# Optimization experiments

Measured on AMD Instinct MI355X. Metric: run time of the kernel, lower is better.

The kernel has to match this reference:

```python
import jax, jax.numpy as jnp
import numpy as np

D_MODEL = 64     # input_dim // 4
D_INNER = 128    # expand * d_model
D_STATE = 16
D_CONV = 4
DT_RANK = 4      # ceil(d_model / 16)
EPS = 1e-5


def layernorm(x, g, b):
    m = x.mean(-1, keepdims=True)
    v = x.var(-1, keepdims=True)
    return (x - m) * jax.lax.rsqrt(v + EPS) * g + b


def mamba(u, W_in, W_conv, b_conv, W_xproj, W_dt, b_dt, A_log, Dp, W_out):
    # u: [B, L, d_model]
    B, L, _ = u.shape
    xz = u @ W_in.T                              # [B, L, 2*d_inner]
    xi, z = xz[..., :D_INNER], xz[..., D_INNER:]
    # depthwise causal conv1d over L
    xp = jnp.pad(xi, ((0, 0), (D_CONV - 1, 0), (0, 0)))
    xc = b_conv + sum(xp[:, k:k + L, :] * W_conv[:, k] for k in range(D_CONV))
    xc = jax.nn.silu(xc)                         # [B, L, d_inner]
    proj = xc @ W_xproj.T                        # [B, L, dt_rank + 2*d_state]
    dtp = proj[..., :DT_RANK]
    Bm = proj[..., DT_RANK:DT_RANK + D_STATE]    # [B, L, d_state]
    Cm = proj[..., DT_RANK + D_STATE:]           # [B, L, d_state]
    dt = jax.nn.softplus(dtp @ W_dt.T + b_dt)    # [B, L, d_inner]
    A = -jnp.exp(A_log)                          # [d_inner, d_state]
    dA = jnp.exp(dt[..., None] * A)              # [B, L, d_inner, d_state]
    dBx = (dt * xc)[..., None] * Bm[:, :, None, :]

    def step(h, t):
        dA_t, dBx_t, C_t = t
        h = dA_t * h + dBx_t                     # [B, d_inner, d_state]
        return h, jnp.einsum('bds,bs->bd', h, C_t)

    h0 = jnp.zeros((B, D_INNER, D_STATE), u.dtype)
    _, ys = jax.lax.scan(step, h0, (dA.transpose(1, 0, 2, 3),
                                    dBx.transpose(1, 0, 2, 3),
                                    Cm.transpose(1, 0, 2)))
    y = ys.transpose(1, 0, 2) + Dp * xc          # [B, L, d_inner]
    y = y * jax.nn.silu(z)
    return y @ W_out.T                           # [B, L, d_model]


def _forward(x, x1, x2, x3, g1, be1, g2, be2, g3, be3, g4, be4, skip_scale,
             W_in, W_conv, b_conv, W_xproj, W_dt, b_dt, A_log, D, W_out):
    Bb, C = x.shape[:2]
    img_dims = x2.shape[2:]
    mparams = (W_in, W_conv, b_conv, W_xproj, W_dt, b_dt, A_log, D, W_out)

    def branch(inp, g, b):
        xf = inp.reshape(Bb, C, -1).transpose(0, 2, 1)   # [B, L, C]
        xn = layernorm(xf, g, b)
        return mamba(xn, *mparams) + skip_scale * xn

    x_mamba = jnp.concatenate([branch(x, g1, be1), branch(x1, g2, be2),
                               branch(x2, g3, be3), branch(x3, g4, be4)], axis=2)
    out = x_mamba.transpose(0, 2, 1).reshape(Bb, 4 * C, *img_dims)
    return out


def setup_inputs():
    key = jax.random.key(0)
    ks = jax.random.split(key, 12)
    f = lambda k, shp, s=1.0: jax.random.normal(k, shp, dtype=jnp.float32) * s
    inp = {
        'x': f(ks[0], (8, 64, 32, 32)),
        'x1': f(ks[1], (8, 64, 32, 32)),
        'x2': f(ks[2], (8, 64, 32, 32)),
        'x3': f(ks[3], (8, 64, 32, 32)),
        'g1': jnp.ones(64), 'be1': jnp.zeros(64),
        'g2': jnp.ones(64), 'be2': jnp.zeros(64),
        'g3': jnp.ones(64), 'be3': jnp.zeros(64),
        'g4': jnp.ones(64), 'be4': jnp.zeros(64),
        'skip_scale': jnp.ones((1,), jnp.float32),
        'W_in': f(ks[4], (2 * D_INNER, D_MODEL), 0.1),
        'W_conv': f(ks[5], (D_INNER, D_CONV), 0.3),
        'b_conv': jnp.zeros(D_INNER),
        'W_xproj': f(ks[6], (DT_RANK + 2 * D_STATE, D_INNER), 0.1),
        'W_dt': f(ks[7], (D_INNER, DT_RANK), 0.1),
        'b_dt': f(ks[8], (D_INNER,), 0.1),
        'A_log': jnp.log(jnp.tile(jnp.arange(1, D_STATE + 1, dtype=jnp.float32), (D_INNER, 1))),
        'D': jnp.ones(D_INNER),
        'W_out': f(ks[9], (D_MODEL, D_INNER), 0.1),
    }
    return inp


def reference(x, x1, x2, x3, g1, be1, g2, be2, g3, be3, g4, be4, skip_scale,
              W_in, W_conv, b_conv, W_xproj, W_dt, b_dt, A_log, D, W_out):
    return _forward(x, x1, x2, x3, g1, be1, g2, be2, g3, be3, g4, be4, skip_scale,
                    W_in, W_conv, b_conv, W_xproj, W_dt, b_dt, A_log, D, W_out)
```

## Files before the change

### kernel.cpp

```cpp
#include <hip/hip_runtime.h>
#include <hip/hip_bf16.h>

#define L2E 1.4426950408889634f
#define LN2 0.6931471805599453f

__device__ __forceinline__ float fexp2(float x) { return __builtin_amdgcn_exp2f(x); }
__device__ __forceinline__ float flog2(float x) { return __builtin_amdgcn_logf(x); }
__device__ __forceinline__ int uniform(int x) { return __builtin_amdgcn_readfirstlane(x); }
__device__ __forceinline__ float sigmoidf_(float v) { return 1.f / (1.f + fexp2(-v * L2E)); }
__device__ __forceinline__ float softplusf_(float t) {
    return (t > 20.f) ? t : LN2 * flog2(1.f + fexp2(t * L2E));
}

constexpr size_t O_M   = 0;
constexpr size_t O_RS  = 32768;
constexpr size_t O_G   = 65536;
constexpr size_t O_Z   = 4259840;
constexpr size_t O_XC  = 8454144;
constexpr size_t O_BM  = 12648448;
constexpr size_t O_CM  = 13172736;
constexpr size_t O_DTP = 13697024;
constexpr size_t O_HP  = 13828096;

__global__ __launch_bounds__(256) void k1_ln_inproj(
    const float* __restrict__ x0, const float* __restrict__ x1,
    const float* __restrict__ x2, const float* __restrict__ x3,
    const float* __restrict__ win,
    const float* __restrict__ g1, const float* __restrict__ be1,
    const float* __restrict__ g2, const float* __restrict__ be2,
    const float* __restrict__ g3, const float* __restrict__ be3,
    const float* __restrict__ g4, const float* __restrict__ be4,
    float* __restrict__ ws)
{
    __shared__ float sX[64 * 68];
    __shared__ float sW[64 * 68];
    __shared__ float sM[64], sR[64];
    int bid = blockIdx.x;
    int seq = bid >> 6, jb = (bid >> 4) & 3, pb = bid & 15;
    int branch = seq >> 3, b = seq & 7;
    int tid = threadIdx.x;
    int lane = tid & 63;
    int wq = uniform(tid >> 6);
    const float* xin = (branch==0)?x0:(branch==1)?x1:(branch==2)?x2:x3;
    const float* gam = (branch==0)?g1:(branch==1)?g2:(branch==2)?g3:g4;
    const float* bet = (branch==0)?be1:(branch==1)?be2:(branch==2)?be3:be4;
    const float* xb = xin + (size_t)b * 65536;

#pragma unroll
    for (int r = 0; r < 16; ++r) {
        int row = r * 4 + wq;
        sX[row * 68 + lane] = xb[(size_t)row * 1024 + pb * 64 + lane];
        sW[lane * 68 + row] = win[(size_t)(jb * 64 + row) * 64 + lane];
    }
    __syncthreads();
    if (tid < 64) {
        float sum = 0.f, sq = 0.f;
#pragma unroll
        for (int c = 0; c < 64; ++c) {
            float v = sX[c * 68 + tid];
            sum += v; sq += v * v;
        }
        float mean = sum * (1.f/64.f);
        float var  = sq * (1.f/64.f) - mean * mean;
        float rs   = rsqrtf(var + 1e-5f);
        sM[tid] = mean; sR[tid] = rs;
        if (jb == 0) {
            ws[O_M  + (size_t)seq * 1024 + pb * 64 + tid] = mean;
            ws[O_RS + (size_t)seq * 1024 + pb * 64 + tid] = rs;
        }
    }
    __syncthreads();
#pragma unroll
    for (int r = 0; r < 16; ++r) {
        int c = r * 4 + wq;
        float v = sX[c * 68 + lane];
        sX[c * 68 + lane] = (v - sM[lane]) * sR[lane] * gam[c] + bet[c];
    }
    __syncthreads();
    int jt = tid >> 4, pt = tid & 15;
    float acc[4][4];
#pragma unroll
    for (int i = 0; i < 4; ++i)
#pragma unroll
        for (int j = 0; j < 4; ++j) acc[i][j] = 0.f;
    for (int c = 0; c < 64; ++c) {
        float4 wv = *(const float4*)&sW[c * 68 + jt * 4];
        float4 xv = *(const float4*)&sX[c * 68 + pt * 4];
        float w[4] = {wv.x, wv.y, wv.z, wv.w};
        float x[4] = {xv.x, xv.y, xv.z, xv.w};
#pragma unroll
        for (int i = 0; i < 4; ++i)
#pragma unroll
            for (int j = 0; j < 4; ++j) acc[i][j] += w[i] * x[j];
    }
    int p0 = pb * 64 + pt * 4;
    float* xi = ws + O_G + (size_t)seq * 131072;
    float* zz = ws + O_Z + (size_t)seq * 131072;
#pragma unroll
    for (int ji = 0; ji < 4; ++ji) {
        int j = jb * 64 + jt * 4 + ji;
        float4 v = make_float4(acc[ji][0], acc[ji][1], acc[ji][2], acc[ji][3]);
        if (j < 128) *(float4*)&xi[(size_t)j * 1024 + p0] = v;
        else         *(float4*)&zz[(size_t)(j - 128) * 1024 + p0] = v;
    }
}

__global__ __launch_bounds__(256) void k2_conv_proj(
    const float* __restrict__ wconv, const float* __restrict__ bconv,
    const float* __restrict__ wxp, float* __restrict__ ws)
{
    __shared__ float sX[128 * 68];
    __shared__ float sWr[4 * 128 * 12];
    int bid = blockIdx.x;
    int seq = bid >> 4, ptile = bid & 15;
    int tid = threadIdx.x;
    int lane = tid & 63;
    int wq = uniform(tid >> 6);
    int p0 = ptile * 64;
    int p  = p0 + lane;
    int j0 = wq * 9;

    const float* xirow = ws + O_G  + (size_t)seq * 131072;
    float*       xcrow = ws + O_XC + (size_t)seq * 131072;

#pragma unroll 4
    for (int r = 0; r < 32; ++r) {
        int d = r * 4 + wq;
        const float* row = xirow + (size_t)d * 1024;
        int gp = p0 - 3 + lane;
        sX[d * 68 + lane] = (gp >= 0) ? row[gp] : 0.f;
        if (lane < 3) sX[d * 68 + 64 + lane] = row[p0 + 61 + lane];
    }
#pragma unroll
    for (int jj = 0; jj < 9; ++jj) {
#pragma unroll
        for (int half = 0; half < 2; ++half) {
            int d = half * 64 + lane;
            sWr[(wq * 128 + d) * 12 + jj] = wxp[(size_t)(j0 + jj) * 128 + d];
        }
    }
    __syncthreads();

#pragma unroll 2
    for (int dd = 0; dd < 32; ++dd) {
        int d = wq * 32 + dd;
        float4 wc = *(const float4*)&wconv[d * 4];
        float v = bconv[d];
        float* rowl = &sX[d * 68];
        v += rowl[lane + 0] * wc.x;
        v += rowl[lane + 1] * wc.y;
        v += rowl[lane + 2] * wc.z;
        v += rowl[lane + 3] * wc.w;
        v = v * sigmoidf_(v);
        xcrow[(size_t)d * 1024 + p] = v;
        rowl[lane + 3] = v;
    }
    __syncthreads();

    float acc[9];
#pragma unroll
    for (int jj = 0; jj < 9; ++jj) acc[jj] = 0.f;
#pragma unroll 4
    for (int d = 0; d < 128; ++d) {
        float xcv = sX[d * 68 + 3 + lane];
        const float* wr = &sWr[(wq * 128 + d) * 12];
        float4 wA = *(const float4*)wr;
        float4 wB = *(const float4*)(wr + 4);
        float  w8 = wr[8];
        acc[0] += wA.x * xcv; acc[1] += wA.y * xcv;
        acc[2] += wA.z * xcv; acc[3] += wA.w * xcv;
        acc[4] += wB.x * xcv; acc[5] += wB.y * xcv;
        acc[6] += wB.z * xcv; acc[7] += wB.w * xcv;
        acc[8] += w8 * xcv;
    }

    float* Bm = ws + O_BM + (size_t)seq * 16384;
    float* Cm = ws + O_CM + (size_t)seq * 16384;
#pragma unroll
    for (int jj = 0; jj < 9; ++jj) {
        int j = j0 + jj;
        float t = acc[jj];
        if (j < 4)       ws[O_DTP + ((size_t)seq * 1024 + p) * 4 + j] = t;
        else if (j < 20) Bm[(size_t)(j - 4)  * 1024 + p] = t;
        else             Cm[(size_t)(j - 20) * 1024 + p] = t;
    }
}

__device__ __forceinline__ void k3_preload(const float* wdt, const float* bdt,
                                           const float* alog, int d0, int s0,
                                           float4& wdt0, float4& wdt1, float& bdt0, float& bdt1,
                                           float* a2)
{
    wdt0 = *(const float4*)(wdt + d0 * 4);
    wdt1 = *(const float4*)(wdt + (d0 + 1) * 4);
    bdt0 = bdt[d0]; bdt1 = bdt[d0 + 1];
    float4 a0 = *(const float4*)(alog + d0 * 16 + s0);
    float4 a1 = *(const float4*)(alog + (d0 + 1) * 16 + s0);
    a2[0] = -fexp2(a0.x * L2E) * L2E; a2[1] = -fexp2(a0.y * L2E) * L2E;
    a2[2] = -fexp2(a0.z * L2E) * L2E; a2[3] = -fexp2(a0.w * L2E) * L2E;
    a2[4] = -fexp2(a1.x * L2E) * L2E; a2[5] = -fexp2(a1.y * L2E) * L2E;
    a2[6] = -fexp2(a1.z * L2E) * L2E; a2[7] = -fexp2(a1.w * L2E) * L2E;
}

__global__ __launch_bounds__(256) void k3a_scan(const float* __restrict__ wdt,
                                                const float* __restrict__ bdt,
                                                const float* __restrict__ alog,
                                                float* __restrict__ ws)
{
    __shared__ float sXC[128 * 33];
    __shared__ __align__(16) float sB[32 * 16];
    __shared__ __align__(16) float sDtp[32 * 4];
    int bid = blockIdx.x;
    int seq = bid >> 5, ch = bid & 31;
    int lb = ch * 32;
    int tid = threadIdx.x;
    int d0 = (tid >> 2) * 2, s0 = (tid & 3) * 4;

    float4 wdt0, wdt1; float bdt0, bdt1; float a2[8];
    k3_preload(wdt, bdt, alog, d0, s0, wdt0, wdt1, bdt0, bdt1, a2);

    const float* xcg = ws + O_XC + (size_t)seq * 131072;
    const float* Bmg = ws + O_BM + (size_t)seq * 16384;
    for (int i = tid; i < 4096; i += 256) {
        int d = i >> 5, li = i & 31;
        sXC[d * 33 + li] = xcg[(size_t)d * 1024 + lb + li];
    }
    for (int i = tid; i < 512; i += 256) {
        int s = i >> 5, li = i & 31;
        sB[li * 16 + s] = Bmg[(size_t)s * 1024 + lb + li];
    }
    if (tid < 128) sDtp[tid] = ws[O_DTP + ((size_t)seq * 1024 + lb + (tid >> 2)) * 4 + (tid & 3)];
    __syncthreads();

    float h[8];
#pragma unroll
    for (int i = 0; i < 8; ++i) h[i] = 0.f;
    float sdt0 = 0.f, sdt1 = 0.f;
    for (int li = 0; li < 32; ++li) {
        float4 q = *(const float4*)&sDtp[li * 4];
        float dt0 = softplusf_(bdt0 + q.x*wdt0.x + q.y*wdt0.y + q.z*wdt0.z + q.w*wdt0.w);
        float dt1 = softplusf_(bdt1 + q.x*wdt1.x + q.y*wdt1.y + q.z*wdt1.z + q.w*wdt1.w);
        float xc0 = sXC[d0 * 33 + li], xc1 = sXC[(d0 + 1) * 33 + li];
        float dx0 = dt0 * xc0, dx1 = dt1 * xc1;
        float4 Bv = *(const float4*)&sB[li * 16 + s0];
        float bv[4] = {Bv.x, Bv.y, Bv.z, Bv.w};
        sdt0 += dt0; sdt1 += dt1;
#pragma unroll
        for (int ss = 0; ss < 4; ++ss) {
            float e0 = fexp2(dt0 * a2[ss]);
            h[ss] = e0 * h[ss] + dx0 * bv[ss];
            float e1 = fexp2(dt1 * a2[4 + ss]);
            h[4 + ss] = e1 * h[4 + ss] + dx1 * bv[ss];
        }
    }
    float* hp = ws + O_HP + (size_t)(seq * 32 + ch) * 4096;
#pragma unroll
    for (int ss = 0; ss < 4; ++ss) {
        hp[d0 * 16 + s0 + ss]            = fexp2(a2[ss] * sdt0);
        hp[(d0 + 1) * 16 + s0 + ss]      = fexp2(a2[4 + ss] * sdt1);
        hp[2048 + d0 * 16 + s0 + ss]     = h[ss];
        hp[2048 + (d0 + 1) * 16 + s0 + ss] = h[4 + ss];
    }
}

__global__ __launch_bounds__(256) void k3b_compose(float* __restrict__ ws)
{
    int seq = blockIdx.x >> 3, dg = blockIdx.x & 7;
    int idx = dg * 256 + threadIdx.x;
    float h = 0.f;
    float* hpb = ws + O_HP + (size_t)seq * 32 * 4096;
    float P = hpb[idx];
    float E = hpb[2048 + idx];
    for (int c = 0; c < 32; ++c) {
        float* hp = hpb + (size_t)c * 4096;
        float Pn = 0.f, En = 0.f;
        if (c < 31) { Pn = hp[4096 + idx]; En = hp[4096 + 2048 + idx]; }
        hp[idx] = h;
        h = P * h + E;
        P = Pn; E = En;
    }
}

__global__ __launch_bounds__(256) void k3cd(
    const float* __restrict__ wdt, const float* __restrict__ bdt,
    const float* __restrict__ alog,
    const float* __restrict__ x0, const float* __restrict__ x1,
    const float* __restrict__ x2, const float* __restrict__ x3,
    const float* __restrict__ g1, const float* __restrict__ be1,
    const float* __restrict__ g2, const float* __restrict__ be2,
    const float* __restrict__ g3, const float* __restrict__ be3,
    const float* __restrict__ g4, const float* __restrict__ be4,
    const float* __restrict__ dpar, const float* __restrict__ woutp,
    const float* __restrict__ skipp, float* __restrict__ ws,
    float* __restrict__ out)
{
    __shared__ float sXC[128 * 33];
    __shared__ __align__(16) float sY[128 * 36];
    __shared__ float sWt[128 * 66];
    __shared__ __align__(16) float sB[32 * 16];
    __shared__ __align__(16) float sC[32 * 16];
    __shared__ __align__(16) float sDtp[32 * 4];
    int bid = blockIdx.x;
    int seq = bid >> 5, ch = bid & 31;
    int branch = seq >> 3, b = seq & 7;
    int lb = ch * 32;
    int tid = threadIdx.x;
    int sq = tid & 3;
    int d0 = (tid >> 2) * 2, s0 = sq * 4;

    float4 wdt0, wdt1; float bdt0, bdt1; float a2[8];
    k3_preload(wdt, bdt, alog, d0, s0, wdt0, wdt1, bdt0, bdt1, a2);

    const float* xcg = ws + O_XC + (size_t)seq * 131072;
    const float* Bmg = ws + O_BM + (size_t)seq * 16384;
    const float* Cmg = ws + O_CM + (size_t)seq * 16384;
    for (int i = tid; i < 4096; i += 256) {
        int d = i >> 5, li = i & 31;
        sXC[d * 33 + li] = xcg[(size_t)d * 1024 + lb + li];
    }
    for (int i = tid; i < 512; i += 256) {
        int s = i >> 5, li = i & 31;
        sB[li * 16 + s] = Bmg[(size_t)s * 1024 + lb + li];
        sC[li * 16 + s] = Cmg[(size_t)s * 1024 + lb + li];
    }
    if (tid < 128) sDtp[tid] = ws[O_DTP + ((size_t)seq * 1024 + lb + (tid >> 2)) * 4 + (tid & 3)];
    for (int i = tid; i < 64 * 128; i += 256) {
        int c = i >> 7, d = i & 127;
        sWt[d * 66 + c] = woutp[i];
    }

    const float* hp = ws + O_HP + (size_t)(seq * 32 + ch) * 4096;
    float4 H0 = *(const float4*)&hp[d0 * 16 + s0];
    float4 H1 = *(const float4*)&hp[(d0 + 1) * 16 + s0];
    float h[8] = {H0.x, H0.y, H0.z, H0.w, H1.x, H1.y, H1.z, H1.w};
    __syncthreads();

    for (int li = 0; li < 32; ++li) {
        float4 q = *(const float4*)&sDtp[li * 4];
        float dt0 = softplusf_(bdt0 + q.x*wdt0.x + q.y*wdt0.y + q.z*wdt0.z + q.w*wdt0.w);
        float dt1 = softplusf_(bdt1 + q.x*wdt1.x + q.y*wdt1.y + q.z*wdt1.z + q.w*wdt1.w);
        float xc0 = sXC[d0 * 33 + li], xc1 = sXC[(d0 + 1) * 33 + li];
        float dx0 = dt0 * xc0, dx1 = dt1 * xc1;
        float4 Bv = *(const float4*)&sB[li * 16 + s0];
        float4 Cv = *(const float4*)&sC[li * 16 + s0];
        float bv[4] = {Bv.x, Bv.y, Bv.z, Bv.w};
        float cv[4] = {Cv.x, Cv.y, Cv.z, Cv.w};
        float acc0 = 0.f, acc1 = 0.f;
#pragma unroll
        for (int ss = 0; ss < 4; ++ss) {
            float e0 = fexp2(dt0 * a2[ss]);
            h[ss] = e0 * h[ss] + dx0 * bv[ss];
            acc0 += h[ss] * cv[ss];
            float e1 = fexp2(dt1 * a2[4 + ss]);
            h[4 + ss] = e1 * h[4 + ss] + dx1 * bv[ss];
            acc1 += h[4 + ss] * cv[ss];
        }
        acc0 += __shfl_xor(acc0, 1); acc0 += __shfl_xor(acc0, 2);
        acc1 += __shfl_xor(acc1, 1); acc1 += __shfl_xor(acc1, 2);
        if (sq == 0) {
            sY[d0 * 36 + li]       = acc0;
            sY[(d0 + 1) * 36 + li] = acc1;
        }
    }
    __syncthreads();

    const float* zzg = ws + O_Z + (size_t)seq * 131072;
    for (int i = tid; i < 4096; i += 256) {
        int d = i >> 5, li = i & 31;
        float zv = zzg[(size_t)d * 1024 + lb + li];
        float yv = sY[d * 36 + li];
        float xcv = sXC[d * 33 + li];
        sY[d * 36 + li] = (yv + dpar[d] * xcv) * (zv * sigmoidf_(zv));
    }
    __syncthreads();

    int ctt = tid >> 3;
    int ptq = tid & 7;
    int c0 = ctt * 2;
    float acc[2][4];
#pragma unroll
    for (int i = 0; i < 2; ++i)
#pragma unroll
        for (int j = 0; j < 4; ++j) acc[i][j] = 0.f;
#pragma unroll 4
    for (int d = 0; d < 128; ++d) {
        float2 wv = *(const float2*)&sWt[d * 66 + c0];
        float4 gv = *(const float4*)&sY[d * 36 + ptq * 4];
        acc[0][0] += wv.x * gv.x; acc[0][1] += wv.x * gv.y;
        acc[0][2] += wv.x * gv.z; acc[0][3] += wv.x * gv.w;
        acc[1][0] += wv.y * gv.x; acc[1][1] += wv.y * gv.y;
        acc[1][2] += wv.y * gv.z; acc[1][3] += wv.y * gv.w;
    }

    const float* xin = (branch==0)?x0:(branch==1)?x1:(branch==2)?x2:x3;
    const float* gam = (branch==0)?g1:(branch==1)?g2:(branch==2)?g3:g4;
    const float* bet = (branch==0)?be1:(branch==1)?be2:(branch==2)?be3:be4;
    const float* xb = xin + (size_t)b * 65536;
    int pp = lb + ptq * 4;
    float skipv = skipp[0];
    float4 m4 = *(const float4*)&ws[O_M  + (size_t)seq * 1024 + pp];
    float4 r4 = *(const float4*)&ws[O_RS + (size_t)seq * 1024 + pp];
    float mm[4] = {m4.x, m4.y, m4.z, m4.w};
    float rr[4] = {r4.x, r4.y, r4.z, r4.w};
#pragma unroll
    for (int ci = 0; ci < 2; ++ci) {
        int c = c0 + ci;
        float4 xv = *(const float4*)&xb[(size_t)c * 1024 + pp];
        float xvv[4] = {xv.x, xv.y, xv.z, xv.w};
        float gc = gam[c], bc = bet[c];
        float o[4];
#pragma unroll
        for (int pi = 0; pi < 4; ++pi) {
            float xn = (xvv[pi] - mm[pi]) * rr[pi] * gc + bc;
            o[pi] = acc[ci][pi] + skipv * xn;
        }
        *(float4*)&out[((size_t)b * 256 + branch * 64 + c) * 1024 + pp] =
            make_float4(o[0], o[1], o[2], o[3]);
    }
}

extern "C" void kernel_launch(void* const* d_in, const int* in_sizes, int n_in,
                              void* d_out, int out_size, void* d_ws, size_t ws_size,
                              hipStream_t stream) {
    float* ws = (float*)d_ws;
    auto f = [&](int i) { return (const float*)d_in[i]; };
    hipLaunchKernelGGL(k1_ln_inproj, dim3(2048), dim3(256), 0, stream,
        f(0), f(1), f(2), f(3), f(13),
        f(4), f(5), f(6), f(7), f(8), f(9), f(10), f(11), ws);
    hipLaunchKernelGGL(k2_conv_proj, dim3(512), dim3(256), 0, stream,
        f(14), f(15), f(16), ws);
    hipLaunchKernelGGL(k3a_scan, dim3(1024), dim3(256), 0, stream, f(17), f(18), f(19), ws);
    hipLaunchKernelGGL(k3b_compose, dim3(256), dim3(256), 0, stream, ws);
    hipLaunchKernelGGL(k3cd, dim3(1024), dim3(256), 0, stream,
        f(17), f(18), f(19),
        f(0), f(1), f(2), f(3),
        f(4), f(5), f(6), f(7), f(8), f(9), f(10), f(11),
        f(20), f(21), f(12), ws, (float*)d_out);
}
```

Measured before the change: 229.3 us.

## Precompute dt and dt*x in conv kernel, stream them into scan kernels

The conv/projection kernel now computes softplus(dt) and dt*xc for every channel and position and writes both to new workspace buffers. The two scan kernels then read these with vector loads instead of staging xc in shared memory and recomputing softplus twice. The output projection reads W_out straight from global memory rather than transposing it into shared memory. This cuts redundant transcendental work and shared memory use, which may raise occupancy, at the cost of about 2×4 MB of extra global traffic.

```diff
diff --git a/kernel.cpp b/kernel.cpp
--- a/kernel.cpp
+++ b/kernel.cpp
@@ -21,6 +21,8 @@
 constexpr size_t O_CM  = 13172736;
 constexpr size_t O_DTP = 13697024;
 constexpr size_t O_HP  = 13828096;
+constexpr size_t O_DT  = 18022400;
+constexpr size_t O_DX  = 22216704;
 
 __global__ __launch_bounds__(256) void k1_ln_inproj(
     const float* __restrict__ x0, const float* __restrict__ x1,
@@ -107,10 +109,13 @@
 
 __global__ __launch_bounds__(256) void k2_conv_proj(
     const float* __restrict__ wconv, const float* __restrict__ bconv,
-    const float* __restrict__ wxp, float* __restrict__ ws)
+    const float* __restrict__ wxp,
+    const float* __restrict__ wdt, const float* __restrict__ bdt,
+    float* __restrict__ ws)
 {
     __shared__ float sX[128 * 68];
     __shared__ float sWr[4 * 128 * 12];
+    __shared__ __align__(16) float sDtp4[64 * 4];
     int bid = blockIdx.x;
     int seq = bid >> 4, ptile = bid & 15;
     int tid = threadIdx.x;
@@ -179,21 +184,32 @@
 #pragma unroll
     for (int jj = 0; jj < 9; ++jj) {
         int j = j0 + jj;
+        if (j < 4) continue;
         float t = acc[jj];
-        if (j < 4)       ws[O_DTP + ((size_t)seq * 1024 + p) * 4 + j] = t;
-        else if (j < 20) Bm[(size_t)(j - 4)  * 1024 + p] = t;
-        else             Cm[(size_t)(j - 20) * 1024 + p] = t;
-    }
-}
-
-__device__ __forceinline__ void k3_preload(const float* wdt, const float* bdt,
-                                           const float* alog, int d0, int s0,
-                                           float4& wdt0, float4& wdt1, float& bdt0, float& bdt1,
-                                           float* a2)
-{
-    wdt0 = *(const float4*)(wdt + d0 * 4);
-    wdt1 = *(const float4*)(wdt + (d0 + 1) * 4);
-    bdt0 = bdt[d0]; bdt1 = bdt[d0 + 1];
+        if (j < 20) Bm[(size_t)(j - 4)  * 1024 + p] = t;
+        else        Cm[(size_t)(j - 20) * 1024 + p] = t;
+    }
+
+    if (wq == 0)
+        *(float4*)&sDtp4[lane * 4] = make_float4(acc[0], acc[1], acc[2], acc[3]);
+    __syncthreads();
+    float* dtg = ws + O_DT + (size_t)seq * 131072;
+    float* dxg = ws + O_DX + (size_t)seq * 131072;
+    float4 qv = *(const float4*)&sDtp4[lane * 4];
+#pragma unroll 4
+    for (int dd = 0; dd < 32; ++dd) {
+        int d = wq * 32 + dd;
+        float4 wv = *(const float4*)&wdt[d * 4];
+        float t = bdt[d] + qv.x*wv.x + qv.y*wv.y + qv.z*wv.z + qv.w*wv.w;
+        float dt = softplusf_(t);
+        float dx = dt * sX[d * 68 + 3 + lane];
+        dtg[(size_t)d * 1024 + p] = dt;
+        dxg[(size_t)d * 1024 + p] = dx;
+    }
+}
+
+__device__ __forceinline__ void a2_preload(const float* alog, int d0, int s0, float* a2)
+{
     float4 a0 = *(const float4*)(alog + d0 * 16 + s0);
     float4 a1 = *(const float4*)(alog + (d0 + 1) * 16 + s0);
     a2[0] = -fexp2(a0.x * L2E) * L2E; a2[1] = -fexp2(a0.y * L2E) * L2E;
@@ -202,63 +218,67 @@
     a2[6] = -fexp2(a1.z * L2E) * L2E; a2[7] = -fexp2(a1.w * L2E) * L2E;
 }
 
-__global__ __launch_bounds__(256) void k3a_scan(const float* __restrict__ wdt,
-                                                const float* __restrict__ bdt,
-                                                const float* __restrict__ alog,
+__global__ __launch_bounds__(256) void k3a_scan(const float* __restrict__ alog,
                                                 float* __restrict__ ws)
 {
-    __shared__ float sXC[128 * 33];
     __shared__ __align__(16) float sB[32 * 16];
-    __shared__ __align__(16) float sDtp[32 * 4];
     int bid = blockIdx.x;
     int seq = bid >> 5, ch = bid & 31;
     int lb = ch * 32;
     int tid = threadIdx.x;
     int d0 = (tid >> 2) * 2, s0 = (tid & 3) * 4;
 
-    float4 wdt0, wdt1; float bdt0, bdt1; float a2[8];
-    k3_preload(wdt, bdt, alog, d0, s0, wdt0, wdt1, bdt0, bdt1, a2);
-
-    const float* xcg = ws + O_XC + (size_t)seq * 131072;
+    float a2[8];
+    a2_preload(alog, d0, s0, a2);
+
     const float* Bmg = ws + O_BM + (size_t)seq * 16384;
-    for (int i = tid; i < 4096; i += 256) {
-        int d = i >> 5, li = i & 31;
-        sXC[d * 33 + li] = xcg[(size_t)d * 1024 + lb + li];
-    }
     for (int i = tid; i < 512; i += 256) {
         int s = i >> 5, li = i & 31;
         sB[li * 16 + s] = Bmg[(size_t)s * 1024 + lb + li];
     }
-    if (tid < 128) sDtp[tid] = ws[O_DTP + ((size_t)seq * 1024 + lb + (tid >> 2)) * 4 + (tid & 3)];
-    __syncthreads();
+    __syncthreads();
+
+    const float* r0t = ws + O_DT + (size_t)seq * 131072 + (size_t)d0 * 1024 + lb;
+    const float* r1t = r0t + 1024;
+    const float* r0x = ws + O_DX + (size_t)seq * 131072 + (size_t)d0 * 1024 + lb;
+    const float* r1x = r0x + 1024;
 
     float h[8];
 #pragma unroll
     for (int i = 0; i < 8; ++i) h[i] = 0.f;
     float sdt0 = 0.f, sdt1 = 0.f;
-    for (int li = 0; li < 32; ++li) {
-        float4 q = *(const float4*)&sDtp[li * 4];
-        float dt0 = softplusf_(bdt0 + q.x*wdt0.x + q.y*wdt0.y + q.z*wdt0.z + q.w*wdt0.w);
-        float dt1 = softplusf_(bdt1 + q.x*wdt1.x + q.y*wdt1.y + q.z*wdt1.z + q.w*wdt1.w);
-        float xc0 = sXC[d0 * 33 + li], xc1 = sXC[(d0 + 1) * 33 + li];
-        float dx0 = dt0 * xc0, dx1 = dt1 * xc1;
-        float4 Bv = *(const float4*)&sB[li * 16 + s0];
-        float bv[4] = {Bv.x, Bv.y, Bv.z, Bv.w};
-        sdt0 += dt0; sdt1 += dt1;
-#pragma unroll
-        for (int ss = 0; ss < 4; ++ss) {
-            float e0 = fexp2(dt0 * a2[ss]);
-            h[ss] = e0 * h[ss] + dx0 * bv[ss];
-            float e1 = fexp2(dt1 * a2[4 + ss]);
-            h[4 + ss] = e1 * h[4 + ss] + dx1 * bv[ss];
+    for (int q4 = 0; q4 < 8; ++q4) {
+        float4 t0 = *(const float4*)&r0t[q4 * 4];
+        float4 t1 = *(const float4*)&r1t[q4 * 4];
+        float4 x0 = *(const float4*)&r0x[q4 * 4];
+        float4 x1 = *(const float4*)&r1x[q4 * 4];
+        float t0a[4] = {t0.x, t0.y, t0.z, t0.w};
+        float t1a[4] = {t1.x, t1.y, t1.z, t1.w};
+        float x0a[4] = {x0.x, x0.y, x0.z, x0.w};
+        float x1a[4] = {x1.x, x1.y, x1.z, x1.w};
+#pragma unroll
+        for (int k = 0; k < 4; ++k) {
+            int li = q4 * 4 + k;
+            float dt0 = t0a[k], dt1 = t1a[k];
+            float dx0 = x0a[k], dx1 = x1a[k];
+            float4 Bv = *(const float4*)&sB[li * 16 + s0];
+            float bv[4] = {Bv.x, Bv.y, Bv.z, Bv.w};
+            sdt0 += dt0; sdt1 += dt1;
+#pragma unroll
+            for (int ss = 0; ss < 4; ++ss) {
+                float e0 = fexp2(dt0 * a2[ss]);
+                h[ss] = e0 * h[ss] + dx0 * bv[ss];
+                float e1 = fexp2(dt1 * a2[4 + ss]);
+                h[4 + ss] = e1 * h[4 + ss] + dx1 * bv[ss];
+            }
         }
     }
     float* hp = ws + O_HP + (size_t)(seq * 32 + ch) * 4096;
 #pragma unroll
     for (int ss = 0; ss < 4; ++ss) {
-        hp[d0 * 16 + s0 + ss]            = fexp2(a2[ss] * sdt0);
-        hp[(d0 + 1) * 16 + s0 + ss]      = fexp2(a2[4 + ss] * sdt1);
-        hp[2048 + d0 * 16 + s0 + ss]     = h[ss];
+        hp[d0 * 16 + s0 + ss]              = fexp2(a2[ss] * sdt0);
+        hp[(d0 + 1) * 16 + s0 + ss]        = fexp2(a2[4 + ss] * sdt1);
+        hp[2048 + d0 * 16 + s0 + ss]       = h[ss];
         hp[2048 + (d0 + 1) * 16 + s0 + ss] = h[4 + ss];
     }
 }
@@ -282,7 +302,6 @@
 }
 
 __global__ __launch_bounds__(256) void k3cd(
-    const float* __restrict__ wdt, const float* __restrict__ bdt,
     const float* __restrict__ alog,
     const float* __restrict__ x0, const float* __restrict__ x1,
     const float* __restrict__ x2, const float* __restrict__ x3,
@@ -294,12 +313,9 @@
     const float* __restrict__ skipp, float* __restrict__ ws,
     float* __restrict__ out)
 {
-    __shared__ float sXC[128 * 33];
     __shared__ __align__(16) float sY[128 * 36];
-    __shared__ float sWt[128 * 66];
     __shared__ __align__(16) float sB[32 * 16];
     __shared__ __align__(16) float sC[32 * 16];
-    __shared__ __align__(16) float sDtp[32 * 4];
     int bid = blockIdx.x;
     int seq = bid >> 5, ch = bid & 31;
     int branch = seq >> 3, b = seq & 7;
@@ -308,26 +324,16 @@
     int sq = tid & 3;
     int d0 = (tid >> 2) * 2, s0 = sq * 4;
 
-    float4 wdt0, wdt1; float bdt0, bdt1; float a2[8];
-    k3_preload(wdt, bdt, alog, d0, s0, wdt0, wdt1, bdt0, bdt1, a2);
-
-    const float* xcg = ws + O_XC + (size_t)seq * 131072;
+    float a2[8];
+    a2_preload(alog, d0, s0, a2);
+
     const float* Bmg = ws + O_BM + (size_t)seq * 16384;
     const float* Cmg = ws + O_CM + (size_t)seq * 16384;
-    for (int i = tid; i < 4096; i += 256) {
-        int d = i >> 5, li = i & 31;
-        sXC[d * 33 + li] = xcg[(size_t)d * 1024 + lb + li];
-    }
     for (int i = tid; i < 512; i += 256) {
         int s = i >> 5, li = i & 31;
         sB[li * 16 + s] = Bmg[(size_t)s * 1024 + lb + li];
         sC[li * 16 + s] = Cmg[(size_t)s * 1024 + lb + li];
     }
-    if (tid < 128) sDtp[tid] = ws[O_DTP + ((size_t)seq * 1024 + lb + (tid >> 2)) * 4 + (tid & 3)];
-    for (int i = tid; i < 64 * 128; i += 256) {
-        int c = i >> 7, d = i & 127;
-        sWt[d * 66 + c] = woutp[i];
-    }
 
     const float* hp = ws + O_HP + (size_t)(seq * 32 + ch) * 4096;
     float4 H0 = *(const float4*)&hp[d0 * 16 + s0];
@@ -335,41 +341,56 @@
     float h[8] = {H0.x, H0.y, H0.z, H0.w, H1.x, H1.y, H1.z, H1.w};
     __syncthreads();
 
-    for (int li = 0; li < 32; ++li) {
-        float4 q = *(const float4*)&sDtp[li * 4];
-        float dt0 = softplusf_(bdt0 + q.x*wdt0.x + q.y*wdt0.y + q.z*wdt0.z + q.w*wdt0.w);
-        float dt1 = softplusf_(bdt1 + q.x*wdt1.x + q.y*wdt1.y + q.z*wdt1.z + q.w*wdt1.w);
-        float xc0 = sXC[d0 * 33 + li], xc1 = sXC[(d0 + 1) * 33 + li];
-        float dx0 = dt0 * xc0, dx1 = dt1 * xc1;
-        float4 Bv = *(const float4*)&sB[li * 16 + s0];
-        float4 Cv = *(const float4*)&sC[li * 16 + s0];
-        float bv[4] = {Bv.x, Bv.y, Bv.z, Bv.w};
-        float cv[4] = {Cv.x, Cv.y, Cv.z, Cv.w};
-        float acc0 = 0.f, acc1 = 0.f;
-#pragma unroll
-        for (int ss = 0; ss < 4; ++ss) {
-            float e0 = fexp2(dt0 * a2[ss]);
-            h[ss] = e0 * h[ss] + dx0 * bv[ss];
-            acc0 += h[ss] * cv[ss];
-            float e1 = fexp2(dt1 * a2[4 + ss]);
-            h[4 + ss] = e1 * h[4 + ss] + dx1 * bv[ss];
-            acc1 += h[4 + ss] * cv[ss];
-        }
-        acc0 += __shfl_xor(acc0, 1); acc0 += __shfl_xor(acc0, 2);
-        acc1 += __shfl_xor(acc1, 1); acc1 += __shfl_xor(acc1, 2);
-        if (sq == 0) {
-            sY[d0 * 36 + li]       = acc0;
-            sY[(d0 + 1) * 36 + li] = acc1;
-        }
-    }
-    __syncthreads();
-
-    const float* zzg = ws + O_Z + (size_t)seq * 131072;
+    const float* r0t = ws + O_DT + (size_t)seq * 131072 + (size_t)d0 * 1024 + lb;
+    const float* r1t = r0t + 1024;
+    const float* r0x = ws + O_DX + (size_t)seq * 131072 + (size_t)d0 * 1024 + lb;
+    const float* r1x = r0x + 1024;
+
+    for (int q4 = 0; q4 < 8; ++q4) {
+        float4 t0 = *(const float4*)&r0t[q4 * 4];
+        float4 t1 = *(const float4*)&r1t[q4 * 4];
+        float4 x0v = *(const float4*)&r0x[q4 * 4];
+        float4 x1v = *(const float4*)&r1x[q4 * 4];
+        float t0a[4] = {t0.x, t0.y, t0.z, t0.w};
+        float t1a[4] = {t1.x, t1.y, t1.z, t1.w};
+        float x0a[4] = {x0v.x, x0v.y, x0v.z, x0v.w};
+        float x1a[4] = {x1v.x, x1v.y, x1v.z, x1v.w};
+#pragma unroll
+        for (int k = 0; k < 4; ++k) {
+            int li = q4 * 4 + k;
+            float dt0 = t0a[k], dt1 = t1a[k];
+            float dx0 = x0a[k], dx1 = x1a[k];
+            float4 Bv = *(const float4*)&sB[li * 16 + s0];
+            float4 Cv = *(const float4*)&sC[li * 16 + s0];
+            float bv[4] = {Bv.x, Bv.y, Bv.z, Bv.w};
+            float cv[4] = {Cv.x, Cv.y, Cv.z, Cv.w};
+            float acc0 = 0.f, acc1 = 0.f;
+#pragma unroll
+            for (int ss = 0; ss < 4; ++ss) {
+                float e0 = fexp2(dt0 * a2[ss]);
+                h[ss] = e0 * h[ss] + dx0 * bv[ss];
+                acc0 += h[ss] * cv[ss];
+                float e1 = fexp2(dt1 * a2[4 + ss]);
+                h[4 + ss] = e1 * h[4 + ss] + dx1 * bv[ss];
+                acc1 += h[4 + ss] * cv[ss];
+            }
+            acc0 += __shfl_xor(acc0, 1); acc0 += __shfl_xor(acc0, 2);
+            acc1 += __shfl_xor(acc1, 1); acc1 += __shfl_xor(acc1, 2);
+            if (sq == 0) {
+                sY[d0 * 36 + li]       = acc0;
+                sY[(d0 + 1) * 36 + li] = acc1;
+            }
+        }
+    }
+    __syncthreads();
+
+    const float* zzg = ws + O_Z  + (size_t)seq * 131072;
+    const float* xcg = ws + O_XC + (size_t)seq * 131072;
     for (int i = tid; i < 4096; i += 256) {
         int d = i >> 5, li = i & 31;
-        float zv = zzg[(size_t)d * 1024 + lb + li];
-        float yv = sY[d * 36 + li];
-        float xcv = sXC[d * 33 + li];
+        float zv  = zzg[(size_t)d * 1024 + lb + li];
+        float xcv = xcg[(size_t)d * 1024 + lb + li];
+        float yv  = sY[d * 36 + li];
         sY[d * 36 + li] = (yv + dpar[d] * xcv) * (zv * sigmoidf_(zv));
     }
     __syncthreads();
@@ -377,19 +398,27 @@
     int ctt = tid >> 3;
     int ptq = tid & 7;
     int c0 = ctt * 2;
+    const float* w0p = woutp + (size_t)c0 * 128;
+    const float* w1p = w0p + 128;
     float acc[2][4];
 #pragma unroll
     for (int i = 0; i < 2; ++i)
 #pragma unroll
         for (int j = 0; j < 4; ++j) acc[i][j] = 0.f;
-#pragma unroll 4
-    for (int d = 0; d < 128; ++d) {
-        float2 wv = *(const float2*)&sWt[d * 66 + c0];
-        float4 gv = *(const float4*)&sY[d * 36 + ptq * 4];
-        acc[0][0] += wv.x * gv.x; acc[0][1] += wv.x * gv.y;
-        acc[0][2] += wv.x * gv.z; acc[0][3] += wv.x * gv.w;
-        acc[1][0] += wv.y * gv.x; acc[1][1] += wv.y * gv.y;
-        acc[1][2] += wv.y * gv.z; acc[1][3] += wv.y * gv.w;
+    for (int d4 = 0; d4 < 32; ++d4) {
+        float4 wa = *(const float4*)&w0p[d4 * 4];
+        float4 wb = *(const float4*)&w1p[d4 * 4];
+        float waa[4] = {wa.x, wa.y, wa.z, wa.w};
+        float wba[4] = {wb.x, wb.y, wb.z, wb.w};
+#pragma unroll
+        for (int k = 0; k < 4; ++k) {
+            int d = d4 * 4 + k;
+            float4 gv = *(const float4*)&sY[d * 36 + ptq * 4];
+            acc[0][0] += waa[k] * gv.x; acc[0][1] += waa[k] * gv.y;
+            acc[0][2] += waa[k] * gv.z; acc[0][3] += waa[k] * gv.w;
+            acc[1][0] += wba[k] * gv.x; acc[1][1] += wba[k] * gv.y;
+            acc[1][2] += wba[k] * gv.z; acc[1][3] += wba[k] * gv.w;
+        }
     }
 
     const float* xin = (branch==0)?x0:(branch==1)?x1:(branch==2)?x2:x3;
@@ -428,11 +457,11 @@
         f(0), f(1), f(2), f(3), f(13),
         f(4), f(5), f(6), f(7), f(8), f(9), f(10), f(11), ws);
     hipLaunchKernelGGL(k2_conv_proj, dim3(512), dim3(256), 0, stream,
-        f(14), f(15), f(16), ws);
-    hipLaunchKernelGGL(k3a_scan, dim3(1024), dim3(256), 0, stream, f(17), f(18), f(19), ws);
+        f(14), f(15), f(16), f(17), f(18), ws);
+    hipLaunchKernelGGL(k3a_scan, dim3(1024), dim3(256), 0, stream, f(19), ws);
     hipLaunchKernelGGL(k3b_compose, dim3(256), dim3(256), 0, stream, ws);
     hipLaunchKernelGGL(k3cd, dim3(1024), dim3(256), 0, stream,
-        f(17), f(18), f(19),
+        f(19),
         f(0), f(1), f(2), f(3),
         f(4), f(5), f(6), f(7), f(8), f(9), f(10), f(11),
         f(20), f(21), f(12), ws, (float*)d_out);
```

Result: faster. 214.1 us (-6.6%).
